# Performance work log

Measured on AMD Instinct MI355X. Metric: run time of the kernel, lower is better.

The kernel has to match this reference:

```python
import jax, jax.numpy as jnp
import numpy as np

B, P, S, D, H = 1, 2048, 2048, 1024, 16
DH = D // H
D_IN, SEQ_LEN = 8, 256  # channel-gate geometry: S = D_IN*SEQ_LEN, pred_len = P//D_IN


def setup_inputs() -> dict:
    key = jax.random.key(0)
    ks = jax.random.split(key, 10)
    n = lambda i, shape, s=1.0: jax.random.normal(ks[i], shape, dtype=jnp.float32) * s
    attn_mask = jnp.tril(jnp.ones((P, S), dtype=bool)).reshape(1, P, 1, S)  # True = attend (causal)
    return {
        "Q": n(0, (B, P, D)),
        "K": n(1, (B, S, D)),
        "V": n(2, (B, S, D)),
        "prev": n(3, (B, P, H, S), 0.1),
        "Wq": n(4, (D, D), 0.02), "bq": jnp.zeros((D,), jnp.float32),
        "Wk": n(5, (D, D), 0.02), "bk": jnp.zeros((D,), jnp.float32),
        "Wv": n(6, (D, D), 0.02), "bv": jnp.zeros((D,), jnp.float32),
        "Wo": n(7, (D, D), 0.02), "bo": jnp.zeros((D,), jnp.float32),
        "ch_gate": n(8, (D_IN, D_IN)),
        "attn_mask": attn_mask,
    }


def reference(Q, K, V, prev, Wq, bq, Wk, bk, Wv, bv, Wo, bo, ch_gate, attn_mask):
    scale = DH ** -0.5
    # qkv projections (nn.Linear: x @ W.T + b), split into heads
    q = (Q @ Wq.T + bq).reshape(B, P, H, DH)
    k = (K @ Wk.T + bk).reshape(B, S, H, DH)
    v = (V @ Wv.T + bv).reshape(B, S, H, DH)
    raw_scores = jnp.einsum('bphd,bshd->bphs', q, k) * scale
    raw_scores = raw_scores + prev  # residual attention
    # channel gate with straight-through estimator
    pred_ch = jnp.arange(P) // (P // D_IN)
    seq_ch = jnp.arange(S) // SEQ_LEN
    s = jax.nn.sigmoid(ch_gate)
    gate_ch = (s >= 0.5).astype(raw_scores.dtype) + s - jax.lax.stop_gradient(s)
    gate_full = gate_ch[pred_ch][:, seq_ch].reshape(1, P, 1, S)
    raw_scores = jnp.where(jnp.isfinite(raw_scores), raw_scores * gate_full, raw_scores)
    # max-stabilized, explicitly masked softmax with mask-based renormalization
    stable = raw_scores - jnp.max(raw_scores, axis=-1, keepdims=True)
    masked = jnp.where(attn_mask, stable, jnp.asarray(-1e9, stable.dtype))
    attn = jax.nn.softmax(masked, axis=-1)
    attn = attn * attn_mask.astype(attn.dtype)
    attn = attn / jnp.clip(jnp.sum(attn, axis=-1, keepdims=True), 1e-9)
    out = jnp.einsum('bphs,bshd->bphd', attn, v).reshape(B, P, H * DH)
    out = out @ Wo.T + bo
    return (out, attn, raw_scores)
```

## Files before the change

### kernel.cpp

```cpp
#include <hip/hip_runtime.h>

#define PP 2048
#define SSEQ 2048
#define DDIM 1024
#define NH 16
#define DH 64

typedef __attribute__((ext_vector_type(4))) float f32x4;
typedef __attribute__((ext_vector_type(8))) short bf16x8;
typedef __attribute__((ext_vector_type(4))) short bf16x4;

__device__ __forceinline__ short f2bf(float f) {
  unsigned u = __builtin_bit_cast(unsigned, f);
  u += 0x7FFFu + ((u >> 16) & 1u);
  return (short)(u >> 16);
}
__device__ __forceinline__ float bf2f(unsigned short u) {
  return __builtin_bit_cast(float, ((unsigned)u) << 16);
}
__device__ __forceinline__ void gld_lds16(const void* g, void* l) {
  __builtin_amdgcn_global_load_lds(
      (const __attribute__((address_space(1))) void*)g,
      (__attribute__((address_space(3))) void*)l, 16, 0, 0);
}

__global__ __launch_bounds__(256) void cvt7(
    const float* __restrict__ s0, const float* __restrict__ s1, const float* __restrict__ s2,
    const float* __restrict__ s3, const float* __restrict__ s4, const float* __restrict__ s5,
    const float* __restrict__ s6,
    unsigned short* __restrict__ d0, unsigned short* __restrict__ d1, unsigned short* __restrict__ d2,
    unsigned short* __restrict__ d3, unsigned short* __restrict__ d4, unsigned short* __restrict__ d5,
    unsigned short* __restrict__ d6) {
  const int z = blockIdx.y;
  const float* s = (z == 0) ? s0 : (z == 1) ? s1 : (z == 2) ? s2 : (z == 3) ? s3
                 : (z == 4) ? s4 : (z == 5) ? s5 : s6;
  unsigned short* d = (z == 0) ? d0 : (z == 1) ? d1 : (z == 2) ? d2 : (z == 3) ? d3
                    : (z == 4) ? d4 : (z == 5) ? d5 : d6;
  const size_t n = (z < 3) ? (size_t)PP * DDIM : (size_t)DDIM * DDIM;
  const size_t i = ((size_t)blockIdx.x * 256 + threadIdx.x) * 8;
  if (i >= n) return;
  const float4 x0 = *(const float4*)(s + i);
  const float4 x1 = *(const float4*)(s + i + 4);
  bf16x8 o;
  o[0] = f2bf(x0.x); o[1] = f2bf(x0.y); o[2] = f2bf(x0.z); o[3] = f2bf(x0.w);
  o[4] = f2bf(x1.x); o[5] = f2bf(x1.y); o[6] = f2bf(x1.z); o[7] = f2bf(x1.w);
  *(bf16x8*)(d + i) = o;
}

template<int YF32>
__device__ __forceinline__ void gemm128_body(
    const unsigned short* __restrict__ A, const unsigned short* __restrict__ B,
    const float* __restrict__ bias, void* __restrict__ Yv) {
  __shared__ unsigned short As[4096];
  __shared__ unsigned short Bs[4096];
  const int tid = threadIdx.x, lane = tid & 63, w = tid >> 6;
  const int m0 = blockIdx.y * 128, n0 = blockIdx.x * 128;
  const int g = lane >> 4, ln = lane & 15;
  const int wm = (w >> 1) * 64, wn = (w & 1) * 64;
  const int sr = tid >> 2, sc = (tid & 3) * 8;
  unsigned short* asd0 = As + w * 512;
  unsigned short* asd1 = As + 2048 + w * 512;
  unsigned short* bsd0 = Bs + w * 512;
  unsigned short* bsd1 = Bs + 2048 + w * 512;
  f32x4 acc[4][4] = {};
  for (int k0 = 0; k0 < DDIM; k0 += 32) {
    __syncthreads();
    gld_lds16(A + (size_t)(m0 + sr) * DDIM + k0 + sc, asd0);
    gld_lds16(A + (size_t)(m0 + 64 + sr) * DDIM + k0 + sc, asd1);
    gld_lds16(B + (size_t)(n0 + sr) * DDIM + k0 + sc, bsd0);
    gld_lds16(B + (size_t)(n0 + 64 + sr) * DDIM + k0 + sc, bsd1);
    __syncthreads();
    bf16x8 a[4], b[4];
#pragma unroll
    for (int mi = 0; mi < 4; ++mi) a[mi] = *(const bf16x8*)&As[(wm + mi * 16 + ln) * 32 + g * 8];
#pragma unroll
    for (int ni = 0; ni < 4; ++ni) b[ni] = *(const bf16x8*)&Bs[(wn + ni * 16 + ln) * 32 + g * 8];
#pragma unroll
    for (int mi = 0; mi < 4; ++mi)
#pragma unroll
      for (int ni = 0; ni < 4; ++ni)
        acc[mi][ni] = __builtin_amdgcn_mfma_f32_16x16x32_bf16(a[mi], b[ni], acc[mi][ni], 0, 0, 0);
  }
#pragma unroll
  for (int mi = 0; mi < 4; ++mi)
#pragma unroll
    for (int ni = 0; ni < 4; ++ni) {
      const int n = n0 + wn + ni * 16 + ln;
      const float bs = bias[n];
#pragma unroll
      for (int r = 0; r < 4; ++r) {
        const int m = m0 + wm + mi * 16 + g * 4 + r;
        const float v = acc[mi][ni][r] + bs;
        if (YF32) ((float*)Yv)[(size_t)m * DDIM + n] = v;
        else ((unsigned short*)Yv)[(size_t)m * DDIM + n] = (unsigned short)f2bf(v);
      }
    }
}

__global__ __launch_bounds__(256, 2) void qkv_gemm(
    const unsigned short* __restrict__ Qb, const unsigned short* __restrict__ Kb,
    const unsigned short* __restrict__ Vb,
    const unsigned short* __restrict__ Wq, const unsigned short* __restrict__ Wk,
    const unsigned short* __restrict__ Wv,
    const float* __restrict__ bq, const float* __restrict__ bk, const float* __restrict__ bv,
    unsigned short* __restrict__ qo, unsigned short* __restrict__ ko,
    unsigned short* __restrict__ vo) {
  const int z = blockIdx.z;
  gemm128_body<0>((z == 0) ? Qb : (z == 1) ? Kb : Vb,
                  (z == 0) ? Wq : (z == 1) ? Wk : Wv,
                  (z == 0) ? bq : (z == 1) ? bk : bv,
                  (z == 0) ? qo : (z == 1) ? ko : vo);
}

__global__ __launch_bounds__(256, 2) void out_gemm(
    const unsigned short* __restrict__ A, const unsigned short* __restrict__ B,
    const float* __restrict__ bias, float* __restrict__ Y) {
  gemm128_body<1>(A, B, bias, Y);
}

__global__ __launch_bounds__(256) void transpose_v(
    const unsigned short* __restrict__ vb, unsigned short* __restrict__ vT) {
  __shared__ unsigned short t[64][72];
  const int tid = threadIdx.x;
  const int sb = blockIdx.x * 64, db = blockIdx.y * 64;
#pragma unroll
  for (int pass = 0; pass < 2; ++pass) {
    const int e = pass * 2048 + tid * 8;
    const int r = e >> 6, c = e & 63;
    *(bf16x8*)&t[r][c] = *(const bf16x8*)(vb + (size_t)(sb + r) * DDIM + db + c);
  }
  __syncthreads();
#pragma unroll
  for (int pass = 0; pass < 2; ++pass) {
    const int e = pass * 2048 + tid * 8;
    const int r = e >> 6, c = e & 63;
    bf16x8 ov;
#pragma unroll
    for (int u = 0; u < 8; ++u) ov[u] = (short)t[c + u][r];
    *(bf16x8*)(vT + (size_t)(db + r) * SSEQ + sb + c) = ov;
  }
}

__global__ __launch_bounds__(256, 2) void scorespv(
    const unsigned short* __restrict__ qb, const unsigned short* __restrict__ kb,
    const unsigned short* __restrict__ vT,
    const float* __restrict__ prev, const float* __restrict__ ch_gate,
    float* __restrict__ raw, float* __restrict__ l_row,
    unsigned short* __restrict__ ctx) {
  __shared__ float Rs[4][16][132];
  __shared__ float lS[4][16];
  __shared__ unsigned short Ks[2][8192];
  const int tid = threadIdx.x, lane = tid & 63, w = tid >> 6;
  const int b = blockIdx.x;
  const int h = (b & 7) * 2 + ((b >> 3) & 1);
  const int pt = b >> 4;
  const int p0 = pt * 64, wr = w * 16;
  const int g = lane >> 4, ln = lane & 15;
  const int myp = p0 + wr + ln;
  const int pc = p0 >> 8;

  const int strow = w * 32 + (lane >> 3);
  const int scol = (((lane & 7) << 4) ^ ((lane >> 3) << 4)) >> 1;

  bf16x8 aq[2];
#pragma unroll
  for (int ks = 0; ks < 2; ++ks)
    aq[ks] = *(const bf16x8*)(qb + (size_t)myp * DDIM + h * DH + ks * 32 + g * 8);

  f32x4 U[4] = {};
  float lsum = 0.f;
  const size_t rowb = ((size_t)myp * NH + h) * SSEQ;

#pragma unroll
  for (int i = 0; i < 4; ++i)
    gld_lds16(kb + (size_t)(strow + i * 8) * DDIM + h * DH + scol,
              &Ks[0][(w * 32 + i * 8) * 64]);
  f32x4 pv[8];
#pragma unroll
  for (int ks = 0; ks < 4; ++ks) {
    pv[2 * ks]     = __builtin_nontemporal_load((const f32x4*)(prev + rowb + ks * 32 + g * 8));
    pv[2 * ks + 1] = __builtin_nontemporal_load((const f32x4*)(prev + rowb + ks * 32 + g * 8 + 4));
  }
  __syncthreads();

  for (int t = 0; t < 16; ++t) {
    const int s0 = t * 128;
    const float gate = (ch_gate[pc * 8 + (s0 >> 8)] >= 0.f) ? 1.f : 0.f;
    if (t < 15) {
#pragma unroll
      for (int i = 0; i < 4; ++i)
        gld_lds16(kb + (size_t)(s0 + 128 + strow + i * 8) * DDIM + h * DH + scol,
                  &Ks[(t + 1) & 1][(w * 32 + i * 8) * 64]);
    }
    const char* Kbuf = (const char*)Ks[t & 1];
#pragma unroll
    for (int half = 0; half < 2; ++half) {
      f32x4 acc[4] = {};
#pragma unroll
      for (int ks = 0; ks < 2; ++ks)
#pragma unroll
        for (int nj = 0; nj < 4; ++nj) {
          const int row = half * 64 + nj * 16 + ln;
          const bf16x8 bk = *(const bf16x8*)(Kbuf + row * 128 + ((ks * 64 + g * 16) ^ ((ln & 7) << 4)));
          acc[nj] = __builtin_amdgcn_mfma_f32_16x16x32_bf16(aq[ks], bk, acc[nj], 0, 0, 0);
        }
#pragma unroll
      for (int nj = 0; nj < 4; ++nj)
#pragma unroll
        for (int r = 0; r < 4; ++r)
          Rs[w][g * 4 + r][half * 64 + nj * 16 + ln] = acc[nj][r];
    }
    f32x4 pvn[8];
    if (t < 15) {
#pragma unroll
      for (int ks = 0; ks < 4; ++ks) {
        pvn[2 * ks]     = __builtin_nontemporal_load((const f32x4*)(prev + rowb + s0 + 128 + ks * 32 + g * 8));
        pvn[2 * ks + 1] = __builtin_nontemporal_load((const f32x4*)(prev + rowb + s0 + 128 + ks * 32 + g * 8 + 4));
      }
    }
    f32x4 v[8];
#pragma unroll
    for (int ks = 0; ks < 4; ++ks)
#pragma unroll
      for (int hf = 0; hf < 2; ++hf) {
        const int c0 = ks * 32 + g * 8 + hf * 4;
        const f32x4 sc = *(const f32x4*)&Rs[w][ln][c0];
        f32x4 vv;
        vv[0] = fmaf(sc[0], 0.125f, pv[ks * 2 + hf][0]) * gate;
        vv[1] = fmaf(sc[1], 0.125f, pv[ks * 2 + hf][1]) * gate;
        vv[2] = fmaf(sc[2], 0.125f, pv[ks * 2 + hf][2]) * gate;
        vv[3] = fmaf(sc[3], 0.125f, pv[ks * 2 + hf][3]) * gate;
        v[ks * 2 + hf] = vv;
        *(f32x4*)(raw + rowb + s0 + c0) = vv;
      }
    if (s0 <= p0 + wr + 15) {
      bf16x8 pa[4];
#pragma unroll
      for (int ks = 0; ks < 4; ++ks) {
        const int cb = s0 + ks * 32 + g * 8;
        float e[8];
#pragma unroll
        for (int j = 0; j < 4; ++j) {
          e[j]     = (cb + j     <= myp) ? __expf(v[2 * ks][j])     : 0.f;
          e[j + 4] = (cb + j + 4 <= myp) ? __expf(v[2 * ks + 1][j]) : 0.f;
        }
        lsum += ((e[0] + e[1]) + (e[2] + e[3])) + ((e[4] + e[5]) + (e[6] + e[7]));
        bf16x8 pk;
#pragma unroll
        for (int j = 0; j < 8; ++j) pk[j] = f2bf(e[j]);
        pa[ks] = pk;
      }
#pragma unroll
      for (int nj = 0; nj < 4; ++nj) {
        const size_t vb0 = (size_t)(h * DH + nj * 16 + ln) * SSEQ + s0;
        const bf16x8 b0 = *(const bf16x8*)(vT + vb0 + g * 8);
        const bf16x8 b1 = *(const bf16x8*)(vT + vb0 + 32 + g * 8);
        const bf16x8 b2 = *(const bf16x8*)(vT + vb0 + 64 + g * 8);
        const bf16x8 b3 = *(const bf16x8*)(vT + vb0 + 96 + g * 8);
        U[nj] = __builtin_amdgcn_mfma_f32_16x16x32_bf16(pa[0], b0, U[nj], 0, 0, 0);
        U[nj] = __builtin_amdgcn_mfma_f32_16x16x32_bf16(pa[1], b1, U[nj], 0, 0, 0);
        U[nj] = __builtin_amdgcn_mfma_f32_16x16x32_bf16(pa[2], b2, U[nj], 0, 0, 0);
        U[nj] = __builtin_amdgcn_mfma_f32_16x16x32_bf16(pa[3], b3, U[nj], 0, 0, 0);
      }
    }
    if (t < 15) {
#pragma unroll
      for (int i = 0; i < 8; ++i) pv[i] = pvn[i];
    }
    __syncthreads();
  }
  lsum += __shfl_xor(lsum, 16);
  lsum += __shfl_xor(lsum, 32);
  if (g == 0) {
    lS[w][ln] = lsum;
    l_row[h * PP + myp] = lsum;
  }
  float il4[4];
#pragma unroll
  for (int r = 0; r < 4; ++r) il4[r] = 1.f / lS[w][g * 4 + r];
#pragma unroll
  for (int nj = 0; nj < 4; ++nj)
#pragma unroll
    for (int r = 0; r < 4; ++r) {
      const int p = p0 + wr + g * 4 + r;
      ctx[(size_t)p * DDIM + h * DH + nj * 16 + ln] = (unsigned short)f2bf(U[nj][r] * il4[r]);
    }
}

__global__ __launch_bounds__(256) void attn_norm(
    const float* __restrict__ raw, const float* __restrict__ l_row,
    float* __restrict__ attn) {
  const int b = blockIdx.x;
  const int lo = b & 255, k8 = b >> 8;
  const int h = lo & 15, ptb = lo >> 4;
  const int pt = ptb + 16 * k8;
  const int p0 = pt * 16;
  __shared__ float ilS[16];
  if (threadIdx.x < 16) ilS[threadIdx.x] = 1.f / l_row[h * PP + p0 + threadIdx.x];
  __syncthreads();
  const int limit = ((p0 + 16 + 127) >> 7) << 7;
  const int col = threadIdx.x * 4;
  for (int c0 = 0; c0 < SSEQ; c0 += 1024) {
    const int c = c0 + col;
#pragma unroll 4
    for (int r = 0; r < 16; ++r) {
      const int p = p0 + r;
      const size_t base = ((size_t)p * NH + h) * SSEQ + c;
      f32x4 av = {0.f, 0.f, 0.f, 0.f};
      if (c < limit) {
        const float il = ilS[r];
        const f32x4 rv = *(const f32x4*)(raw + base);
        av[0] = (c + 0 <= p) ? __expf(rv[0]) * il : 0.f;
        av[1] = (c + 1 <= p) ? __expf(rv[1]) * il : 0.f;
        av[2] = (c + 2 <= p) ? __expf(rv[2]) * il : 0.f;
        av[3] = (c + 3 <= p) ? __expf(rv[3]) * il : 0.f;
      }
      __builtin_nontemporal_store(av, (f32x4*)(attn + base));
    }
  }
}

extern "C" void kernel_launch(void* const* d_in, const int* in_sizes, int n_in,
                              void* d_out, int out_size, void* d_ws, size_t ws_size,
                              hipStream_t stream) {
  (void)in_sizes; (void)n_in; (void)out_size; (void)ws_size;
  const float* Q    = (const float*)d_in[0];
  const float* K    = (const float*)d_in[1];
  const float* V    = (const float*)d_in[2];
  const float* prev = (const float*)d_in[3];
  const float* Wq   = (const float*)d_in[4];
  const float* bq   = (const float*)d_in[5];
  const float* Wk   = (const float*)d_in[6];
  const float* bk   = (const float*)d_in[7];
  const float* Wv   = (const float*)d_in[8];
  const float* bv   = (const float*)d_in[9];
  const float* Wo   = (const float*)d_in[10];
  const float* bo   = (const float*)d_in[11];
  const float* ch_gate = (const float*)d_in[12];

  float* out  = (float*)d_out;
  float* attn = out + (size_t)PP * DDIM;
  float* raw  = attn + (size_t)PP * NH * SSEQ;

  unsigned short* ws16 = (unsigned short*)d_ws;
  unsigned short* qb   = ws16;
  unsigned short* kb   = qb + 2097152;
  unsigned short* vb   = kb + 2097152;
  unsigned short* vT   = vb + 2097152;
  unsigned short* buf5 = vT + 2097152;
  unsigned short* buf6 = buf5 + 2097152;
  unsigned short* buf7 = buf6 + 2097152;
  float* l_row = (float*)(buf7 + 2097152);
  unsigned short* wqb = (unsigned short*)(l_row + 32768);
  unsigned short* wkb = wqb + 1048576;
  unsigned short* wvb = wkb + 1048576;
  unsigned short* wob = wvb + 1048576;

  unsigned short* Qbf = buf5;
  unsigned short* Kbf = buf6;
  unsigned short* Vbf = buf7;
  unsigned short* ctx = buf5;

  dim3 blk(256);
  cvt7<<<dim3(1024, 7), blk, 0, stream>>>(
      Q, K, V, Wq, Wk, Wv, Wo, Qbf, Kbf, Vbf, wqb, wkb, wvb, wob);
  qkv_gemm<<<dim3(DDIM / 128, PP / 128, 3), blk, 0, stream>>>(
      Qbf, Kbf, Vbf, wqb, wkb, wvb, bq, bk, bv, qb, kb, vb);
  transpose_v<<<dim3(SSEQ / 64, DDIM / 64), blk, 0, stream>>>(vb, vT);
  scorespv<<<dim3(512), blk, 0, stream>>>(
      qb, kb, vT, prev, ch_gate, raw, l_row, ctx);
  attn_norm<<<dim3(2048), blk, 0, stream>>>(raw, l_row, attn);
  out_gemm<<<dim3(DDIM / 128, PP / 128), blk, 0, stream>>>(ctx, wob, bo, out);
}
```

Baseline: 285.9 us.

## Halve score staging LDS, fuse epilogue per half, raise occupancy to 3

The score tile is now staged through LDS one 64-column half at a time, and the scale/prev/gate epilogue plus the exp and bf16 packing run right after each half's MFMAs. The Rs buffer shrinks to half its size, the prev prefetch is issued earlier, and launch bounds ask for 3 blocks per SM instead of 2. The aim is more resident waves to hide the memory-bound prev/raw traffic, with lower LDS and register use per block. The cost is a tighter register budget, which may cause spills, and extra same-wave LDS reuse across the two halves.

New measurement: 293.7 us. +2.7%, slower.

```diff
diff --git a/kernel.cpp b/kernel.cpp
--- a/kernel.cpp
+++ b/kernel.cpp
@@ -141,13 +141,13 @@
   }
 }
 
-__global__ __launch_bounds__(256, 2) void scorespv(
+__global__ __launch_bounds__(256, 3) void scorespv(
     const unsigned short* __restrict__ qb, const unsigned short* __restrict__ kb,
     const unsigned short* __restrict__ vT,
     const float* __restrict__ prev, const float* __restrict__ ch_gate,
     float* __restrict__ raw, float* __restrict__ l_row,
     unsigned short* __restrict__ ctx) {
-  __shared__ float Rs[4][16][132];
+  __shared__ float Rs[4][16][68];
   __shared__ float lS[4][16];
   __shared__ unsigned short Ks[2][8192];
   const int tid = threadIdx.x, lane = tid & 63, w = tid >> 6;
@@ -192,7 +192,17 @@
         gld_lds16(kb + (size_t)(s0 + 128 + strow + i * 8) * DDIM + h * DH + scol,
                   &Ks[(t + 1) & 1][(w * 32 + i * 8) * 64]);
     }
+    f32x4 pvn[8];
+    if (t < 15) {
+#pragma unroll
+      for (int ks = 0; ks < 4; ++ks) {
+        pvn[2 * ks]     = __builtin_nontemporal_load((const f32x4*)(prev + rowb + s0 + 128 + ks * 32 + g * 8));
+        pvn[2 * ks + 1] = __builtin_nontemporal_load((const f32x4*)(prev + rowb + s0 + 128 + ks * 32 + g * 8 + 4));
+      }
+    }
     const char* Kbuf = (const char*)Ks[t & 1];
+    const bool causal = (s0 <= p0 + wr + 15);
+    bf16x8 pa[4];
 #pragma unroll
     for (int half = 0; half < 2; ++half) {
       f32x4 acc[4] = {};
@@ -208,48 +218,39 @@
       for (int nj = 0; nj < 4; ++nj)
 #pragma unroll
         for (int r = 0; r < 4; ++r)
-          Rs[w][g * 4 + r][half * 64 + nj * 16 + ln] = acc[nj][r];
-    }
-    f32x4 pvn[8];
-    if (t < 15) {
-#pragma unroll
-      for (int ks = 0; ks < 4; ++ks) {
-        pvn[2 * ks]     = __builtin_nontemporal_load((const f32x4*)(prev + rowb + s0 + 128 + ks * 32 + g * 8));
-        pvn[2 * ks + 1] = __builtin_nontemporal_load((const f32x4*)(prev + rowb + s0 + 128 + ks * 32 + g * 8 + 4));
-      }
-    }
-    f32x4 v[8];
-#pragma unroll
-    for (int ks = 0; ks < 4; ++ks)
-#pragma unroll
-      for (int hf = 0; hf < 2; ++hf) {
-        const int c0 = ks * 32 + g * 8 + hf * 4;
-        const f32x4 sc = *(const f32x4*)&Rs[w][ln][c0];
-        f32x4 vv;
-        vv[0] = fmaf(sc[0], 0.125f, pv[ks * 2 + hf][0]) * gate;
-        vv[1] = fmaf(sc[1], 0.125f, pv[ks * 2 + hf][1]) * gate;
-        vv[2] = fmaf(sc[2], 0.125f, pv[ks * 2 + hf][2]) * gate;
-        vv[3] = fmaf(sc[3], 0.125f, pv[ks * 2 + hf][3]) * gate;
-        v[ks * 2 + hf] = vv;
-        *(f32x4*)(raw + rowb + s0 + c0) = vv;
-      }
-    if (s0 <= p0 + wr + 15) {
-      bf16x8 pa[4];
-#pragma unroll
-      for (int ks = 0; ks < 4; ++ks) {
-        const int cb = s0 + ks * 32 + g * 8;
+          Rs[w][g * 4 + r][nj * 16 + ln] = acc[nj][r];
+#pragma unroll
+      for (int ks2 = 0; ks2 < 2; ++ks2) {
+        const int kglob = half * 2 + ks2;
         float e[8];
 #pragma unroll
-        for (int j = 0; j < 4; ++j) {
-          e[j]     = (cb + j     <= myp) ? __expf(v[2 * ks][j])     : 0.f;
-          e[j + 4] = (cb + j + 4 <= myp) ? __expf(v[2 * ks + 1][j]) : 0.f;
+        for (int hf = 0; hf < 2; ++hf) {
+          const int ch = ks2 * 32 + g * 8 + hf * 4;
+          const int c0 = half * 64 + ch;
+          const f32x4 sc = *(const f32x4*)&Rs[w][ln][ch];
+          f32x4 vv;
+          vv[0] = fmaf(sc[0], 0.125f, pv[kglob * 2 + hf][0]) * gate;
+          vv[1] = fmaf(sc[1], 0.125f, pv[kglob * 2 + hf][1]) * gate;
+          vv[2] = fmaf(sc[2], 0.125f, pv[kglob * 2 + hf][2]) * gate;
+          vv[3] = fmaf(sc[3], 0.125f, pv[kglob * 2 + hf][3]) * gate;
+          *(f32x4*)(raw + rowb + s0 + c0) = vv;
+          if (causal) {
+            const int cb = s0 + c0;
+#pragma unroll
+            for (int j = 0; j < 4; ++j)
+              e[hf * 4 + j] = (cb + j <= myp) ? __expf(vv[j]) : 0.f;
+          }
         }
-        lsum += ((e[0] + e[1]) + (e[2] + e[3])) + ((e[4] + e[5]) + (e[6] + e[7]));
-        bf16x8 pk;
-#pragma unroll
-        for (int j = 0; j < 8; ++j) pk[j] = f2bf(e[j]);
-        pa[ks] = pk;
-      }
+        if (causal) {
+          lsum += ((e[0] + e[1]) + (e[2] + e[3])) + ((e[4] + e[5]) + (e[6] + e[7]));
+          bf16x8 pk;
+#pragma unroll
+          for (int j = 0; j < 8; ++j) pk[j] = f2bf(e[j]);
+          pa[kglob] = pk;
+        }
+      }
+    }
+    if (causal) {
 #pragma unroll
       for (int nj = 0; nj < 4; ++nj) {
         const size_t vb0 = (size_t)(h * DH + nj * 16 + ln) * SSEQ + s0;
```
